# Optimization experiments

Measured on AMD Instinct MI355X. Metric: run time of the kernel, lower is better.

The kernel has to match this reference:

```python
import jax, jax.numpy as jnp
import numpy as np

WIN = 7          # window_size (square)
N = WIN * WIN    # tokens per window = 49
C = 384          # channels
H = 12           # heads
HD = C // H      # head dim = 32
NW = 4           # shifted-window mask groups
BW = 4096        # total windows (batch*num_windows)
SCALE = HD ** -0.5


def _relative_position_index():
    coords_h = np.arange(WIN)
    coords_w = np.arange(WIN)
    coords = np.stack(np.meshgrid(coords_h, coords_w, indexing='ij'))  # [2,7,7]
    cf = coords.reshape(2, -1)                                         # [2,49]
    rel = cf[:, :, None] - cf[:, None, :]                              # [2,49,49]
    rel = rel.transpose(1, 2, 0)
    rel[:, :, 0] += WIN - 1
    rel[:, :, 1] += WIN - 1
    rel[:, :, 0] *= 2 * WIN - 1
    return rel.sum(-1).astype(np.int32)                                # [49,49]


def setup_inputs() -> dict:
    key = jax.random.key(0)
    ks = jax.random.split(key, 7)
    x = jax.random.normal(ks[0], (BW, N, C), dtype=jnp.float32)
    mask = jax.random.normal(ks[1], (NW, N, N), dtype=jnp.float32)
    w_qkv = jax.random.normal(ks[2], (C, 3 * C), dtype=jnp.float32) * 0.02
    b_qkv = jnp.zeros((3 * C,), dtype=jnp.float32)
    bias_table = jax.random.normal(ks[3], ((2 * WIN - 1) ** 2, H), dtype=jnp.float32) * 0.02
    w_proj = jax.random.normal(ks[4], (C, C), dtype=jnp.float32) * 0.02
    b_proj = jnp.zeros((C,), dtype=jnp.float32)
    rel_index = jnp.asarray(_relative_position_index())
    return {"x": x, "mask": mask, "w_qkv": w_qkv, "b_qkv": b_qkv,
            "bias_table": bias_table, "w_proj": w_proj, "b_proj": b_proj,
            "rel_index": rel_index}


def reference(x, mask, w_qkv, b_qkv, bias_table, w_proj, b_proj, rel_index):
    B = x.shape[0]
    # QKV projection: [B,N,3C] -> [3,B,H,N,hd]
    qkv = x @ w_qkv + b_qkv
    qkv = qkv.reshape(B, N, 3, H, HD).transpose(2, 0, 3, 1, 4)
    q, k, v = qkv[0], qkv[1], qkv[2]
    q = q * SCALE
    attn = jnp.einsum('bhnd,bhmd->bhnm', q, k)          # [B,H,N,N]
    # gathered relative position bias: [N,N,H] -> [H,N,N]
    bias = bias_table[rel_index]                         # [N,N,H]
    attn = attn + bias.transpose(2, 0, 1)[None]
    # shift-window mask add
    attn = attn.reshape(B // NW, NW, H, N, N) + mask[None, :, None]
    attn = attn.reshape(B, H, N, N)
    attn = jax.nn.softmax(attn, axis=-1)
    out = jnp.einsum('bhnm,bhmd->bhnd', attn, v)         # [B,H,N,hd]
    out = out.transpose(0, 2, 1, 3).reshape(B, N, C)
    out = out @ w_proj + b_proj
    return out
```

## Files before the change

### kernel.cpp

```cpp
#include <hip/hip_runtime.h>

typedef unsigned short u16;
typedef u16 u16x4 __attribute__((ext_vector_type(4)));
typedef u16 u16x8 __attribute__((ext_vector_type(8)));
typedef __bf16 bf16x8 __attribute__((ext_vector_type(8)));
typedef float f32x4 __attribute__((ext_vector_type(4)));

#define MFMA16 __builtin_amdgcn_mfma_f32_16x16x32_bf16
#define QSCALE 0.17677669529663689f
#define VMWAIT(N) asm volatile("s_waitcnt vmcnt(" #N ")" ::: "memory")

__device__ __forceinline__ u16 f2bf(float f) {
  unsigned u = __builtin_bit_cast(unsigned, f);
  u += 0x7fffu + ((u >> 16) & 1u);
  return (u16)(u >> 16);
}
__device__ __forceinline__ bf16x8 as_bf(u16x8 u) { return __builtin_bit_cast(bf16x8, u); }
__device__ __forceinline__ f32x4 zf4() { f32x4 z = {0.f, 0.f, 0.f, 0.f}; return z; }

template <int CTRL>
__device__ __forceinline__ float dppf(float x) {
  int i = __builtin_bit_cast(int, x);
  int r = __builtin_amdgcn_update_dpp(i, i, CTRL, 0xf, 0xf, false);
  return __builtin_bit_cast(float, r);
}
__device__ __forceinline__ float rmax16(float x) {
  x = fmaxf(x, dppf<0xB1>(x));
  x = fmaxf(x, dppf<0x4E>(x));
  x = fmaxf(x, dppf<0x124>(x));
  x = fmaxf(x, dppf<0x128>(x));
  return x;
}
__device__ __forceinline__ float rsum16(float x) {
  x += dppf<0xB1>(x);
  x += dppf<0x4E>(x);
  x += dppf<0x124>(x);
  x += dppf<0x128>(x);
  return x;
}

__global__ __launch_bounds__(256) void prep_kernel(
    const float* __restrict__ wq, const float* __restrict__ wp,
    const float* __restrict__ bt, const int* __restrict__ ri,
    const float* __restrict__ mask,
    u16* __restrict__ wqT, u16* __restrict__ wpT, float* __restrict__ smask2) {
  int idx = blockIdx.x * 256 + threadIdx.x;
  if (idx < 442368) {
    int nn = idx / 384, kk = idx % 384;
    wqT[idx] = f2bf(wq[(size_t)kk * 1152 + nn]);
  } else if (idx < 589824) {
    int i2 = idx - 442368;
    int nn = i2 / 384, kk = i2 % 384;
    wpT[i2] = f2bf(wp[(size_t)kk * 384 + nn]);
  } else if (idx < 740352) {
    int i3 = idx - 589824;
    int g = i3 / 37632;
    int rem = i3 % 37632;
    int h = rem / 3136;
    int nm = rem % 3136;
    int n = nm >> 6;
    int r2 = nm & 63;
    int lane = r2 >> 2, nj = r2 & 3;
    int m = nj * 16 + lane;
    float v = 0.f;
    if (m < 49 && n < 49)
      v = bt[ri[n * 49 + m] * 12 + h] + mask[g * 2401 + n * 49 + m];
    smask2[i3] = v;
  }
}

__global__ __launch_bounds__(256) void conv_x(const float* __restrict__ x,
                                              u16* __restrict__ xb) {
  size_t i = ((size_t)blockIdx.x * 256 + threadIdx.x) * 8;
  f32x4 a = *(const f32x4*)(x + i);
  f32x4 b = *(const f32x4*)(x + i + 4);
  u16x8 o;
  o[0] = f2bf(a[0]); o[1] = f2bf(a[1]); o[2] = f2bf(a[2]); o[3] = f2bf(a[3]);
  o[4] = f2bf(b[0]); o[5] = f2bf(b[1]); o[6] = f2bf(b[2]); o[7] = f2bf(b[3]);
  *(u16x8*)(xb + i) = o;
}

template <int NCH, bool QKV>
__global__ __launch_bounds__(256) void gemm4(
    const u16* __restrict__ Wt, const u16* __restrict__ Xb,
    const float* __restrict__ bias, void* __restrict__ outp) {
  __shared__ u16 As[2][128 * 32];
  __shared__ u16 Bs[2][128 * 32];
  const int t = threadIdx.x;
  const int l = t & 63, w = t >> 6;

  const int bid = blockIdx.x;
  const int xcd = bid & 7, q = bid >> 3;
  const int logical = xcd * (196 * NCH) + q;
  const int tokt = logical / NCH, cht = logical % NCH;
  const int tb = tokt * 128;
  const int cb = cht * 128;
  const int LDC = NCH * 128;

  f32x4 acc[4][4];
#pragma unroll
  for (int mi = 0; mi < 4; ++mi)
#pragma unroll
    for (int ni = 0; ni < 4; ++ni) acc[mi][ni] = zf4();

  const int rA = (w >> 1) * 64 + (l & 15);
  const int rB = (w & 1) * 64 + (l & 15);
  const int gsel = l >> 4;
  const int gA = ((gsel ^ ((rA >> 1) & 3))) * 8;
  const int gB = ((gsel ^ ((rB >> 1) & 3))) * 8;

  auto stage = [&](int bf, int kt) {
    const int ko = kt * 32;
#pragma unroll
    for (int j = 0; j < 2; ++j) {
      const int gi = j * 256 + t;
      const int row = gi >> 2, slot = gi & 3;
      const int sg = (slot ^ ((row >> 1) & 3)) * 8;
      __builtin_amdgcn_global_load_lds(
          (const __attribute__((address_space(1))) unsigned int*)
              (Wt + (size_t)(cb + row) * 384 + ko + sg),
          (__attribute__((address_space(3))) unsigned int*)(&As[bf][gi * 8]),
          16, 0, 0);
      __builtin_amdgcn_global_load_lds(
          (const __attribute__((address_space(1))) unsigned int*)
              (Xb + (size_t)(tb + row) * 384 + ko + sg),
          (__attribute__((address_space(3))) unsigned int*)(&Bs[bf][gi * 8]),
          16, 0, 0);
    }
  };

  auto kbody = [&](int cur, int ktnext, bool dostage) {
    __builtin_amdgcn_sched_barrier(0);
    __builtin_amdgcn_s_barrier();
    bf16x8 af[4], bfr[4];
#pragma unroll
    for (int mi = 0; mi < 4; ++mi)
      af[mi] = *(const bf16x8*)(&As[cur][(rA + mi * 16) * 32 + gA]);
#pragma unroll
    for (int nj = 0; nj < 4; ++nj)
      bfr[nj] = *(const bf16x8*)(&Bs[cur][(rB + nj * 16) * 32 + gB]);
    asm volatile("s_waitcnt lgkmcnt(0)" ::: "memory");
    __builtin_amdgcn_sched_barrier(0);
    __builtin_amdgcn_s_barrier();
    if (dostage) stage(cur, ktnext);
    __builtin_amdgcn_sched_barrier(0);
    __builtin_amdgcn_s_setprio(1);
#pragma unroll
    for (int mi = 0; mi < 4; ++mi)
#pragma unroll
      for (int nj = 0; nj < 4; ++nj)
        acc[mi][nj] = MFMA16(af[mi], bfr[nj], acc[mi][nj], 0, 0, 0);
    __builtin_amdgcn_s_setprio(0);
  };

  stage(0, 0);
  stage(1, 1);
#pragma unroll
  for (int kt = 0; kt < 10; ++kt) {
    VMWAIT(4);
    kbody(kt & 1, kt + 2, true);
  }
  VMWAIT(4);
  kbody(0, 0, false);
  VMWAIT(0);
  kbody(1, 0, false);

#pragma unroll
  for (int mi = 0; mi < 4; ++mi) {
    const int ch = cb + (w >> 1) * 64 + mi * 16 + (l >> 4) * 4;
    const f32x4 bv = *(const f32x4*)(bias + ch);
#pragma unroll
    for (int nj = 0; nj < 4; ++nj) {
      const int tok = tb + (w & 1) * 64 + nj * 16 + (l & 15);
      if constexpr (QKV) {
        const float scl = (ch < 384) ? QSCALE : 1.0f;
        u16x4 pk;
#pragma unroll
        for (int r = 0; r < 4; ++r) pk[r] = f2bf((acc[mi][nj][r] + bv[r]) * scl);
        *(u16x4*)((u16*)outp + (size_t)tok * LDC + ch) = pk;
      } else {
        f32x4 o;
#pragma unroll
        for (int r = 0; r < 4; ++r) o[r] = acc[mi][nj][r] + bv[r];
        *(f32x4*)((float*)outp + (size_t)tok * LDC + ch) = o;
      }
    }
  }
}

__global__ __launch_bounds__(768, 3) void attn_kernel(
    const u16* __restrict__ qkvb, const float* __restrict__ smask2,
    u16* __restrict__ attnb) {
  __shared__ u16 Pl[12][4096];
  __shared__ u16 Vt[12][2336];
  const int t = threadIdx.x;
  const int l = t & 63, wv = t >> 6;
  const int bid = blockIdx.x;
  const int b = (bid & 7) * 512 + (bid >> 3);
  const int h = wv;
  u16* Pw = &Pl[wv][0];
  u16* Vw = &Vt[wv][0];
  const u16x8 z = {0, 0, 0, 0, 0, 0, 0, 0};

#pragma unroll
  for (int i = 0; i < 4; ++i) {
    const int row = i * 16 + (l >> 2);
    const int sg = l & 3;
    u16x8 vv = z;
    if (row < 49)
      vv = *(const u16x8*)(qkvb + (size_t)(b * 49 + row) * 1152 + 768 + h * 32 + sg * 8);
#pragma unroll
    for (int e = 0; e < 8; ++e) {
      const int d = sg * 8 + e;
      Vw[d * 72 + (d >> 3) * 8 + row] = vv[e];
    }
  }

  const u16* base = qkvb + (size_t)b * 49 * 1152 + h * 32 + (l >> 4) * 8;
  bf16x8 qa[4], kb[4];
#pragma unroll
  for (int mi = 0; mi < 4; ++mi) {
    const int n = mi * 16 + (l & 15);
    qa[mi] = (n < 49) ? *(const bf16x8*)(base + (size_t)n * 1152) : as_bf(z);
    kb[mi] = (n < 49) ? *(const bf16x8*)(base + 384 + (size_t)n * 1152) : as_bf(z);
  }

  f32x4 s[4][4];
  __builtin_amdgcn_s_setprio(1);
#pragma unroll
  for (int mi = 0; mi < 4; ++mi)
#pragma unroll
    for (int nj = 0; nj < 4; ++nj) s[mi][nj] = MFMA16(qa[mi], kb[nj], zf4(), 0, 0, 0);
  __builtin_amdgcn_s_setprio(0);

  const float* sm2 = smask2 + ((size_t)(b & 3) * 12 + h) * 3136;
#pragma unroll
  for (int mi = 0; mi < 4; ++mi) {
#pragma unroll
    for (int r = 0; r < 4; ++r) {
      const int n = mi * 16 + (l >> 4) * 4 + r;
      if (n < 49) {
        const f32x4 bv = *(const f32x4*)(sm2 + n * 64 + (l & 15) * 4);
        s[mi][0][r] += bv[0];
        s[mi][1][r] += bv[1];
        s[mi][2][r] += bv[2];
        s[mi][3][r] = ((l & 15) == 0) ? s[mi][3][r] + bv[3] : -1e30f;
      }
    }
  }
#pragma unroll
  for (int mi = 0; mi < 4; ++mi) {
#pragma unroll
    for (int r = 0; r < 4; ++r) {
      float mx = fmaxf(fmaxf(s[mi][0][r], s[mi][1][r]), fmaxf(s[mi][2][r], s[mi][3][r]));
      mx = rmax16(mx);
      float e0 = 0.f;
#pragma unroll
      for (int nj = 0; nj < 4; ++nj) {
        const float p = __expf(s[mi][nj][r] - mx);
        s[mi][nj][r] = p;
        e0 += p;
      }
      e0 = rsum16(e0);
      const float inv = 1.0f / e0;
#pragma unroll
      for (int nj = 0; nj < 4; ++nj) s[mi][nj][r] *= inv;
    }
  }
#pragma unroll
  for (int mi = 0; mi < 4; ++mi)
#pragma unroll
    for (int r = 0; r < 4; ++r) {
      const int row = mi * 16 + (l >> 4) * 4 + r;
#pragma unroll
      for (int nj = 0; nj < 4; ++nj) {
        const int col = nj * 16 + (l & 15);
        Pw[row * 64 + (((col >> 3) ^ (row & 7)) * 8) + (col & 7)] = f2bf(s[mi][nj][r]);
      }
    }
  asm volatile("s_waitcnt lgkmcnt(0)" ::: "memory");
  __builtin_amdgcn_sched_barrier(0);

  f32x4 ot[2][4];
#pragma unroll
  for (int dj = 0; dj < 2; ++dj)
#pragma unroll
    for (int mi = 0; mi < 4; ++mi) ot[dj][mi] = zf4();
#pragma unroll
  for (int ks = 0; ks < 2; ++ks) {
    bf16x8 va[2], pb[4];
#pragma unroll
    for (int dj = 0; dj < 2; ++dj) {
      const int d0 = dj * 16 + (l & 15);
      va[dj] = *(const bf16x8*)(Vw + d0 * 72 + (d0 >> 3) * 8 + ks * 32 + (l >> 4) * 8);
    }
#pragma unroll
    for (int mi = 0; mi < 4; ++mi) {
      const int row = mi * 16 + (l & 15);
      pb[mi] = *(const bf16x8*)(Pw + row * 64 + (((ks * 4 + (l >> 4)) ^ (l & 7)) * 8));
    }
    __builtin_amdgcn_s_setprio(1);
#pragma unroll
    for (int dj = 0; dj < 2; ++dj)
#pragma unroll
      for (int mi = 0; mi < 4; ++mi)
        ot[dj][mi] = MFMA16(va[dj], pb[mi], ot[dj][mi], 0, 0, 0);
    __builtin_amdgcn_s_setprio(0);
  }
#pragma unroll
  for (int dj = 0; dj < 2; ++dj)
#pragma unroll
    for (int mi = 0; mi < 4; ++mi) {
      const int n = mi * 16 + (l & 15);
      if (n < 49) {
        u16x4 pk;
        pk[0] = f2bf(ot[dj][mi][0]);
        pk[1] = f2bf(ot[dj][mi][1]);
        pk[2] = f2bf(ot[dj][mi][2]);
        pk[3] = f2bf(ot[dj][mi][3]);
        *(u16x4*)(attnb + (size_t)(b * 49 + n) * 384 + h * 32 + dj * 16 + (l >> 4) * 4) = pk;
      }
    }
}

extern "C" void kernel_launch(void* const* d_in, const int* in_sizes, int n_in,
                              void* d_out, int out_size, void* d_ws, size_t ws_size,
                              hipStream_t stream) {
  const float* x       = (const float*)d_in[0];
  const float* mask    = (const float*)d_in[1];
  const float* w_qkv   = (const float*)d_in[2];
  const float* b_qkv   = (const float*)d_in[3];
  const float* bias_t  = (const float*)d_in[4];
  const float* w_proj  = (const float*)d_in[5];
  const float* b_proj  = (const float*)d_in[6];
  const int*   rel_idx = (const int*)d_in[7];
  float* out = (float*)d_out;

  char* ws = (char*)d_ws;
  u16*   wqT    = (u16*)ws;
  u16*   wpT    = (u16*)(ws + 884736);
  float* smask2 = (float*)(ws + 1179648);
  u16*   qkvb   = (u16*)(ws + 1781760);
  u16*   xb     = (u16*)(ws + 464203776);
  u16*   attnb  = (u16*)(ws + 464203776);

  prep_kernel<<<2892, 256, 0, stream>>>(w_qkv, w_proj, bias_t, rel_idx, mask,
                                        wqT, wpT, smask2);
  conv_x<<<37632, 256, 0, stream>>>(x, xb);
  gemm4<9, true><<<14112, 256, 0, stream>>>(wqT, xb, b_qkv, qkvb);
  attn_kernel<<<4096, 768, 0, stream>>>(qkvb, smask2, attnb);
  gemm4<3, false><<<4704, 256, 0, stream>>>(wpT, attnb, b_proj, out);
}
```

Before: 809.1 us.

## Fuse output projection into attention kernel and triple-buffer QKV GEMM

The output projection GEMM now runs inside the attention kernel. Each window's attention output is written to LDS in a swizzled layout, and the 12 waves then compute the 49x384 projection with MFMA, reading the transposed projection weights from global memory. This removes the bf16 attention-output round trip through HBM and one kernel launch, at the cost of extra syncthreads and per-block weight reads. Separately, the QKV GEMM goes from double-buffered to triple-buffered LDS staging with deeper vmcnt waits, to hide more global load latency at the cost of more shared memory.

New measurement: 862.8 us. 6.6% more time.

```diff
diff --git a/kernel.cpp b/kernel.cpp
--- a/kernel.cpp
+++ b/kernel.cpp
@@ -81,11 +81,11 @@
 }
 
 template <int NCH, bool QKV>
-__global__ __launch_bounds__(256) void gemm4(
+__global__ __launch_bounds__(256) void gemm6(
     const u16* __restrict__ Wt, const u16* __restrict__ Xb,
     const float* __restrict__ bias, void* __restrict__ outp) {
-  __shared__ u16 As[2][128 * 32];
-  __shared__ u16 Bs[2][128 * 32];
+  __shared__ u16 As[3][128 * 32];
+  __shared__ u16 Bs[3][128 * 32];
   const int t = threadIdx.x;
   const int l = t & 63, w = t >> 6;
 
@@ -155,15 +155,18 @@
 
   stage(0, 0);
   stage(1, 1);
-#pragma unroll
-  for (int kt = 0; kt < 10; ++kt) {
-    VMWAIT(4);
-    kbody(kt & 1, kt + 2, true);
-  }
+  stage(2, 2);
+#pragma unroll
+  for (int kt = 0; kt < 9; ++kt) {
+    VMWAIT(8);
+    kbody(kt % 3, kt + 3, true);
+  }
+  VMWAIT(8);
+  kbody(0, 0, false);
   VMWAIT(4);
-  kbody(0, 0, false);
+  kbody(1, 0, false);
   VMWAIT(0);
-  kbody(1, 0, false);
+  kbody(2, 0, false);
 
 #pragma unroll
   for (int mi = 0; mi < 4; ++mi) {
@@ -188,9 +191,10 @@
   }
 }
 
-__global__ __launch_bounds__(768, 3) void attn_kernel(
+__global__ __launch_bounds__(768, 3) void attn_proj_kernel(
     const u16* __restrict__ qkvb, const float* __restrict__ smask2,
-    u16* __restrict__ attnb) {
+    const u16* __restrict__ wpT, const float* __restrict__ bproj,
+    float* __restrict__ out) {
   __shared__ u16 Pl[12][4096];
   __shared__ u16 Vt[12][2336];
   const int t = threadIdx.x;
@@ -200,6 +204,7 @@
   const int h = wv;
   u16* Pw = &Pl[wv][0];
   u16* Vw = &Vt[wv][0];
+  u16* Ost = &Pl[0][0];
   const u16x8 z = {0, 0, 0, 0, 0, 0, 0, 0};
 
 #pragma unroll
@@ -307,20 +312,69 @@
         ot[dj][mi] = MFMA16(va[dj], pb[mi], ot[dj][mi], 0, 0, 0);
     __builtin_amdgcn_s_setprio(0);
   }
+
+  __syncthreads();
+
 #pragma unroll
   for (int dj = 0; dj < 2; ++dj)
 #pragma unroll
     for (int mi = 0; mi < 4; ++mi) {
       const int n = mi * 16 + (l & 15);
       if (n < 49) {
+        const int k0 = wv * 32 + dj * 16 + (l >> 4) * 4;
+        const int g = k0 >> 3;
+        const int swg = (g & ~7) | ((g & 7) ^ (n & 7));
         u16x4 pk;
         pk[0] = f2bf(ot[dj][mi][0]);
         pk[1] = f2bf(ot[dj][mi][1]);
         pk[2] = f2bf(ot[dj][mi][2]);
         pk[3] = f2bf(ot[dj][mi][3]);
-        *(u16x4*)(attnb + (size_t)(b * 49 + n) * 384 + h * 32 + dj * 16 + (l >> 4) * 4) = pk;
-      }
-    }
+        *(u16x4*)(Ost + n * 384 + swg * 8 + (k0 & 7)) = pk;
+      }
+    }
+  __syncthreads();
+
+  f32x4 pacc[2][4];
+#pragma unroll
+  for (int mi = 0; mi < 2; ++mi)
+#pragma unroll
+    for (int nj = 0; nj < 4; ++nj) pacc[mi][nj] = zf4();
+#pragma unroll
+  for (int ks = 0; ks < 12; ++ks) {
+    bf16x8 wa[2], ob[4];
+#pragma unroll
+    for (int mi = 0; mi < 2; ++mi)
+      wa[mi] = *(const bf16x8*)(wpT + (size_t)(wv * 32 + mi * 16 + (l & 15)) * 384 + ks * 32 + (l >> 4) * 8);
+#pragma unroll
+    for (int nj = 0; nj < 4; ++nj) {
+      const int tok = nj * 16 + (l & 15);
+      const int g = ks * 4 + (l >> 4);
+      const int swg = (g & ~7) | ((g & 7) ^ (tok & 7));
+      ob[nj] = *(const bf16x8*)(Ost + tok * 384 + swg * 8);
+    }
+    __builtin_amdgcn_s_setprio(1);
+#pragma unroll
+    for (int mi = 0; mi < 2; ++mi)
+#pragma unroll
+      for (int nj = 0; nj < 4; ++nj)
+        pacc[mi][nj] = MFMA16(wa[mi], ob[nj], pacc[mi][nj], 0, 0, 0);
+    __builtin_amdgcn_s_setprio(0);
+  }
+#pragma unroll
+  for (int mi = 0; mi < 2; ++mi) {
+    const int ch = wv * 32 + mi * 16 + (l >> 4) * 4;
+    const f32x4 bv = *(const f32x4*)(bproj + ch);
+#pragma unroll
+    for (int nj = 0; nj < 4; ++nj) {
+      const int tok = nj * 16 + (l & 15);
+      if (tok < 49) {
+        f32x4 o;
+#pragma unroll
+        for (int r = 0; r < 4; ++r) o[r] = pacc[mi][nj][r] + bv[r];
+        *(f32x4*)(out + (size_t)(b * 49 + tok) * 384 + ch) = o;
+      }
+    }
+  }
 }
 
 extern "C" void kernel_launch(void* const* d_in, const int* in_sizes, int n_in,
@@ -342,12 +396,10 @@
   float* smask2 = (float*)(ws + 1179648);
   u16*   qkvb   = (u16*)(ws + 1781760);
   u16*   xb     = (u16*)(ws + 464203776);
-  u16*   attnb  = (u16*)(ws + 464203776);
 
   prep_kernel<<<2892, 256, 0, stream>>>(w_qkv, w_proj, bias_t, rel_idx, mask,
                                         wqT, wpT, smask2);
   conv_x<<<37632, 256, 0, stream>>>(x, xb);
-  gemm4<9, true><<<14112, 256, 0, stream>>>(wqT, xb, b_qkv, qkvb);
-  attn_kernel<<<4096, 768, 0, stream>>>(qkvb, smask2, attnb);
-  gemm4<3, false><<<4704, 256, 0, stream>>>(wpT, attnb, b_proj, out);
-}
+  gemm6<9, true><<<14112, 256, 0, stream>>>(wqT, xb, b_qkv, qkvb);
+  attn_proj_kernel<<<4096, 768, 0, stream>>>(qkvb, smask2, wpT, b_proj, out);
+}
```
